# Performance work log

Hardware: AMD Instinct MI355X
Metric: run time of the kernel (lower is better)

Reference implementation:

```python
import jax, jax.numpy as jnp
import numpy as np


def setup_inputs() -> dict:
    key = jax.random.key(0)
    k1, k2 = jax.random.split(key)
    N, D, E = 16384, 4096, 64  # tokens, n_embd, n_exp
    x = jax.random.normal(k1, (N, D), dtype=jnp.float32)
    W = jax.random.normal(k2, (E, D), dtype=jnp.float32) * 0.02  # w_gate weight [n_exp, n_embd]
    return {"x": x, "W": W, "top_k": 4, "n_groups": 8, "n_limited_groups": 4}


def reference(x, W, top_k, n_groups, n_limited_groups):
    ROUTE_SCALE = 1.0
    N = x.shape[0]
    E = W.shape[0]
    exp_per_group = E // n_groups

    logits = x @ W.T                      # [N, E] gate linear (bias=False)
    scores = jax.nn.softmax(logits, -1)   # func == 'softmax'

    # group-limited routing: pick top n_limited_groups groups by max score (bias=False path)
    gs = scores.reshape(N, n_groups, exp_per_group)
    group_scores = gs.max(axis=-1)                             # [N, G]
    _, top_grp = jax.lax.top_k(group_scores, n_limited_groups)  # [N, L]
    selected = jnp.any(
        jnp.arange(n_groups)[None, None, :] == top_grp[:, :, None], axis=1
    )                                                           # [N, G] bool
    masked = jnp.where(selected[:, :, None], gs, -jnp.inf).reshape(N, E)

    # top-k experts over unmasked scores; weights are the gathered scores
    topk_vals, topk_idx = jax.lax.top_k(masked, top_k)          # [N, K]
    weights = (topk_vals * ROUTE_SCALE).astype(x.dtype)         # softmax -> no renorm

    # histc over expert ids
    counts = jnp.zeros((E,), jnp.int32).at[topk_idx.reshape(-1)].add(1)
    return weights, topk_idx, counts
```

## Files before the change

kernel.cpp:

```cpp
#include <hip/hip_runtime.h>
#include <math.h>

#define NTOK 16384
#define DDIM 4096
#define NEXP 64
#define KTOP 4

#define SPLITK 16
#define KPER (DDIM / SPLITK)
#define BK 32
#define NSTG (KPER / BK)
#define WROWS 16
#define NWAVE 4
#define TPB (WROWS * NWAVE)
#define NBLK ((NTOK / TPB) * SPLITK)

typedef __attribute__((ext_vector_type(8))) short short8;
typedef __attribute__((ext_vector_type(4))) float f32x4;


__device__ __forceinline__ unsigned short f2bf_rtn(float x) {
    unsigned int b = __float_as_uint(x);
    return (unsigned short)((b + 0x7FFFu + ((b >> 16) & 1u)) >> 16);
}
__device__ __forceinline__ float bf2f(unsigned short h) {
    return __uint_as_float(((unsigned int)h) << 16);
}
__device__ __forceinline__ short8 mk8(unsigned int a, unsigned int b,
                                      unsigned int c, unsigned int d) {
    union { unsigned int u[4]; short8 s; } p;
    p.u[0] = a; p.u[1] = b; p.u[2] = c; p.u[3] = d;
    return p.s;
}
__device__ __forceinline__ void gl2lds16(const void* g, void* l) {
    __builtin_amdgcn_global_load_lds(
        (const __attribute__((address_space(1))) unsigned int*)g,
        (__attribute__((address_space(3))) unsigned int*)l, 16, 0, 0);
}

__global__ __launch_bounds__(256) void prep_kernel(
    const float* __restrict__ W, unsigned short* __restrict__ Whi,
    unsigned short* __restrict__ Wlo, float* __restrict__ counts)
{
    int idx = blockIdx.x * 256 + threadIdx.x;
    float x = W[idx];
    unsigned short h = f2bf_rtn(x);
    float lo = x - bf2f(h);
    Whi[idx] = h;
    Wlo[idx] = f2bf_rtn(lo);
    if (blockIdx.x == 0 && threadIdx.x < NEXP) counts[threadIdx.x] = 0.0f;
}

__global__ __launch_bounds__(256, 2) void gemm_kernel(
    const float* __restrict__ X, const unsigned short* __restrict__ Whi,
    const unsigned short* __restrict__ Wlo, float* __restrict__ part)
{
    __shared__ unsigned short sH[NEXP * KPER];
    __shared__ unsigned short sL[NEXP * KPER];
    __shared__ float sXa[NWAVE][2][WROWS * BK];

    const int tid  = threadIdx.x;
    const int lane = tid & 63;
    const int w    = tid >> 6;
    const int tb   = blockIdx.x >> 4;
    const int s    = blockIdx.x & 15;
    const int kbase = s * KPER;
    const int wtok  = tb * TPB + w * WROWS;

    #pragma unroll
    for (int i = 0; i < 8; ++i) {
        const int g  = i * 256 + tid;
        const int e  = g >> 5;
        const int p  = g & 31;
        const int gb = (i * 256 + (tid >> 6) * 64) * 8;
        const size_t src = (size_t)e * DDIM + kbase + ((p ^ (e & 7)) << 3);
        gl2lds16(Whi + src, &sH[gb]);
        gl2lds16(Wlo + src, &sL[gb]);
    }

    const int xrow = (lane >> 3);
    const int xp   = lane & 7;
    const float* xsrc0 = X + (size_t)(wtok + xrow) * DDIM + kbase
                       + ((xp ^ (xrow & 7)) << 2);
    const float* xsrc1 = X + (size_t)(wtok + 8 + xrow) * DDIM + kbase
                       + ((xp ^ ((xrow + 8) & 7)) << 2);
    float* const xb0 = &sXa[w][0][0];
    float* const xb1 = &sXa[w][1][0];

#define ISSUE_X(buf, st)                                                    \
    {                                                                       \
        gl2lds16(xsrc0 + (st) * BK, (buf));                                 \
        gl2lds16(xsrc1 + (st) * BK, (buf) + 256);                           \
    }

    ISSUE_X(xb0, 0)
    ISSUE_X(xb1, 1)
    __syncthreads();

    const int fr = lane & 15;
    const int fg = lane >> 4;
    const int xkey = fr & 7;

    f32x4 acc[4];
    #pragma unroll
    for (int ng = 0; ng < 4; ++ng) acc[ng] = (f32x4){0.f, 0.f, 0.f, 0.f};

    #pragma unroll
    for (int st = 0; st < NSTG; ++st) {
        if (st < NSTG - 1) {
            asm volatile("s_waitcnt vmcnt(2)" ::: "memory");
        } else {
            asm volatile("s_waitcnt vmcnt(0)" ::: "memory");
        }
        __builtin_amdgcn_sched_barrier(0);

        const float* cx = (st & 1) ? xb1 : xb0;

        const float4 qa = *(const float4*)&cx[fr * BK + (((fg * 2    ) ^ xkey) << 2)];
        const float4 qb = *(const float4*)&cx[fr * BK + (((fg * 2 + 1) ^ xkey) << 2)];

        const unsigned int u0 = __float_as_uint(qa.x), u1 = __float_as_uint(qa.y);
        const unsigned int u2 = __float_as_uint(qa.z), u3 = __float_as_uint(qa.w);
        const unsigned int u4 = __float_as_uint(qb.x), u5 = __float_as_uint(qb.y);
        const unsigned int u6 = __float_as_uint(qb.z), u7 = __float_as_uint(qb.w);
        const short8 ahi = mk8((u0 >> 16) | (u1 & 0xFFFF0000u),
                               (u2 >> 16) | (u3 & 0xFFFF0000u),
                               (u4 >> 16) | (u5 & 0xFFFF0000u),
                               (u6 >> 16) | (u7 & 0xFFFF0000u));
        const float l0 = qa.x - __uint_as_float(u0 & 0xFFFF0000u);
        const float l1 = qa.y - __uint_as_float(u1 & 0xFFFF0000u);
        const float l2 = qa.z - __uint_as_float(u2 & 0xFFFF0000u);
        const float l3 = qa.w - __uint_as_float(u3 & 0xFFFF0000u);
        const float l4 = qb.x - __uint_as_float(u4 & 0xFFFF0000u);
        const float l5 = qb.y - __uint_as_float(u5 & 0xFFFF0000u);
        const float l6 = qb.z - __uint_as_float(u6 & 0xFFFF0000u);
        const float l7 = qb.w - __uint_as_float(u7 & 0xFFFF0000u);
        const short8 alo = mk8(
            (__float_as_uint(l0) >> 16) | (__float_as_uint(l1) & 0xFFFF0000u),
            (__float_as_uint(l2) >> 16) | (__float_as_uint(l3) & 0xFFFF0000u),
            (__float_as_uint(l4) >> 16) | (__float_as_uint(l5) & 0xFFFF0000u),
            (__float_as_uint(l6) >> 16) | (__float_as_uint(l7) & 0xFFFF0000u));

        #pragma unroll
        for (int ng = 0; ng < 4; ++ng) {
            const int e  = ng * 16 + fr;
            const int so = e * KPER + (((st * 4 + fg) ^ xkey) << 3);
            const short8 bh = *(const short8*)&sH[so];
            const short8 bl = *(const short8*)&sL[so];
            acc[ng] = __builtin_amdgcn_mfma_f32_16x16x32_bf16(ahi, bh, acc[ng], 0, 0, 0);
            acc[ng] = __builtin_amdgcn_mfma_f32_16x16x32_bf16(ahi, bl, acc[ng], 0, 0, 0);
            acc[ng] = __builtin_amdgcn_mfma_f32_16x16x32_bf16(alo, bh, acc[ng], 0, 0, 0);
        }

        if (st + 2 < NSTG) {
            asm volatile("s_waitcnt lgkmcnt(0)" ::: "memory");
            __builtin_amdgcn_sched_barrier(0);
            float* nb = (st & 1) ? xb1 : xb0;
            ISSUE_X(nb, st + 2)
        }
    }
#undef ISSUE_X

    #pragma unroll
    for (int r = 0; r < 4; ++r) {
        const int n = wtok + fg * 4 + r;
        float* __restrict__ pp = part + ((size_t)n * SPLITK + s) * NEXP;
        #pragma unroll
        for (int ng = 0; ng < 4; ++ng)
            pp[ng * 16 + fr] = acc[ng][r];
    }
}

__global__ __launch_bounds__(256) void route_kernel(
    const float* __restrict__ part, float* __restrict__ outW,
    float* __restrict__ outI, float* __restrict__ counts)
{
    __shared__ int hist[NEXP];
    const int tid = threadIdx.x;
    if (tid < NEXP) hist[tid] = 0;
    __syncthreads();

    const int lane = tid & 63;
    const int wv   = tid >> 6;
    const int tok_base = blockIdx.x * 32 + wv * 8;

    for (int t = 0; t < 8; ++t) {
        const int n = tok_base + t;
        float L = 0.0f;
        #pragma unroll
        for (int s = 0; s < SPLITK; ++s)
            L += part[((size_t)n * SPLITK + s) * NEXP + lane];

        float m = L;
        #pragma unroll
        for (int off = 32; off > 0; off >>= 1) m = fmaxf(m, __shfl_xor(m, off));
        float p = expf(L - m);
        float ssum = p;
        #pragma unroll
        for (int off = 32; off > 0; off >>= 1) ssum += __shfl_xor(ssum, off);
        const float score = p / ssum;

        float gm = score;
        gm = fmaxf(gm, __shfl_xor(gm, 1));
        gm = fmaxf(gm, __shfl_xor(gm, 2));
        gm = fmaxf(gm, __shfl_xor(gm, 4));

        float ga[8];
        #pragma unroll
        for (int g = 0; g < 8; ++g) ga[g] = __shfl(gm, g * 8);
        unsigned selmask = 0u;
        #pragma unroll
        for (int r = 0; r < 4; ++r) {
            float best = -INFINITY; int bg = 0;
            #pragma unroll
            for (int g = 0; g < 8; ++g) {
                bool taken  = (selmask >> g) & 1u;
                bool better = (!taken) && (ga[g] > best);
                bg   = better ? g : bg;
                best = better ? ga[g] : best;
            }
            selmask |= (1u << bg);
        }

        float ms = ((selmask >> (lane >> 3)) & 1u) ? score : -INFINITY;
        float wk[4]; int wi[4];
        #pragma unroll
        for (int r = 0; r < 4; ++r) {
            float v = ms; int ix = lane;
            #pragma unroll
            for (int off = 32; off > 0; off >>= 1) {
                float vo = __shfl_xor(v, off);
                int   io = __shfl_xor(ix, off);
                if (vo > v || (vo == v && io < ix)) { v = vo; ix = io; }
            }
            wk[r] = v; wi[r] = ix;
            if (lane == ix) ms = -INFINITY;
        }

        if (lane == 0) {
            *(float4*)&outW[(size_t)n * 4] = make_float4(wk[0], wk[1], wk[2], wk[3]);
            *(float4*)&outI[(size_t)n * 4] =
                make_float4((float)wi[0], (float)wi[1], (float)wi[2], (float)wi[3]);
            atomicAdd(&hist[wi[0]], 1);
            atomicAdd(&hist[wi[1]], 1);
            atomicAdd(&hist[wi[2]], 1);
            atomicAdd(&hist[wi[3]], 1);
        }
    }

    __syncthreads();
    if (tid < NEXP) atomicAdd(&counts[tid], (float)hist[tid]);
}

extern "C" void kernel_launch(void* const* d_in, const int* in_sizes, int n_in,
                              void* d_out, int out_size, void* d_ws, size_t ws_size,
                              hipStream_t stream) {
    const float* X = (const float*)d_in[0];
    const float* W = (const float*)d_in[1];

    float* outW   = (float*)d_out;
    float* outI   = outW + (size_t)NTOK * KTOP;
    float* counts = outW + (size_t)2 * NTOK * KTOP;

    float*          part = (float*)d_ws;
    unsigned short* Whi  = (unsigned short*)(part + (size_t)NTOK * SPLITK * NEXP);
    unsigned short* Wlo  = Whi + (size_t)NEXP * DDIM;

    prep_kernel<<<(NEXP * DDIM) / 256, 256, 0, stream>>>(W, Whi, Wlo, counts);
    gemm_kernel<<<NBLK, 256, 0, stream>>>(X, Whi, Wlo, part);
    route_kernel<<<NTOK / 32, 256, 0, stream>>>(part, outW, outI, counts);
}
```

Measured before the change: 115.1 us.

## Stream W slices per stage with triple-buffered block-shared LDS and fewer split-K partitions

Instead of preloading a whole 64x256 W slice (hi/lo bf16) into LDS per block, the GEMM now streams 32-wide W and X tiles per stage into a three-slot ring shared by all 8 waves, with a block barrier each stage. Split-K drops from 16 to 4, and blocks grow to 512 threads covering 128 tokens. This cuts LDS footprint and the prologue load, shrinks the partial-sum buffer and route-kernel reduction, and amortizes each W tile over more tokens. In exchange it adds a per-stage __syncthreads-style barrier and relies on hand-tuned vmcnt counts being correct.

New measurement: 108.2 us. -6.0%, faster.

```diff
diff --git a/kernel.cpp b/kernel.cpp
--- a/kernel.cpp
+++ b/kernel.cpp
@@ -6,13 +6,11 @@
 #define NEXP 64
 #define KTOP 4
 
-#define SPLITK 16
+#define SPLITK 4
 #define KPER (DDIM / SPLITK)
 #define BK 32
 #define NSTG (KPER / BK)
-#define WROWS 16
-#define NWAVE 4
-#define TPB (WROWS * NWAVE)
+#define TPB 128
 #define NBLK ((NTOK / TPB) * SPLITK)
 
 typedef __attribute__((ext_vector_type(8))) short short8;
@@ -51,55 +49,52 @@
     if (blockIdx.x == 0 && threadIdx.x < NEXP) counts[threadIdx.x] = 0.0f;
 }
 
-__global__ __launch_bounds__(256, 2) void gemm_kernel(
+__global__ __launch_bounds__(512, 4) void gemm_kernel(
     const float* __restrict__ X, const unsigned short* __restrict__ Whi,
     const unsigned short* __restrict__ Wlo, float* __restrict__ part)
 {
-    __shared__ unsigned short sH[NEXP * KPER];
-    __shared__ unsigned short sL[NEXP * KPER];
-    __shared__ float sXa[NWAVE][2][WROWS * BK];
+    __shared__ float          sX[3][TPB * BK];
+    __shared__ unsigned short sH[3][NEXP * BK];
+    __shared__ unsigned short sL[3][NEXP * BK];
 
     const int tid  = threadIdx.x;
     const int lane = tid & 63;
     const int w    = tid >> 6;
-    const int tb   = blockIdx.x >> 4;
-    const int s    = blockIdx.x & 15;
+    const int tb   = blockIdx.x >> 2;
+    const int s    = blockIdx.x & 3;
     const int kbase = s * KPER;
-    const int wtok  = tb * TPB + w * WROWS;
-
-    #pragma unroll
-    for (int i = 0; i < 8; ++i) {
-        const int g  = i * 256 + tid;
-        const int e  = g >> 5;
-        const int p  = g & 31;
-        const int gb = (i * 256 + (tid >> 6) * 64) * 8;
-        const size_t src = (size_t)e * DDIM + kbase + ((p ^ (e & 7)) << 3);
-        gl2lds16(Whi + src, &sH[gb]);
-        gl2lds16(Wlo + src, &sL[gb]);
-    }
-
-    const int xrow = (lane >> 3);
-    const int xp   = lane & 7;
-    const float* xsrc0 = X + (size_t)(wtok + xrow) * DDIM + kbase
-                       + ((xp ^ (xrow & 7)) << 2);
-    const float* xsrc1 = X + (size_t)(wtok + 8 + xrow) * DDIM + kbase
-                       + ((xp ^ ((xrow + 8) & 7)) << 2);
-    float* const xb0 = &sXa[w][0][0];
-    float* const xb1 = &sXa[w][1][0];
-
-#define ISSUE_X(buf, st)                                                    \
+    const int tok0 = tb * TPB;
+
+    const int r0 = (w * 2    ) * 8 + (lane >> 3);
+    const int r1 = (w * 2 + 1) * 8 + (lane >> 3);
+    const int xp = lane & 7;
+    const float* xsrc0 = X + (size_t)(tok0 + r0) * DDIM + kbase + ((xp ^ (r0 & 7)) << 2);
+    const float* xsrc1 = X + (size_t)(tok0 + r1) * DDIM + kbase + ((xp ^ (r1 & 7)) << 2);
+    const int xdst0 = (w * 2    ) * 256;
+    const int xdst1 = (w * 2 + 1) * 256;
+
+    const unsigned short* const wtab_src = (w < 4) ? Whi : Wlo;
+    const int eb = w & 3;
+    const int we = eb * 16 + (lane & 15);
+    const unsigned short* wsrc = wtab_src + (size_t)we * DDIM + kbase + (lane >> 4) * 8;
+    const int wdst = eb * 512 + lane * 8;
+    unsigned short (* const wtab_dst)[NEXP * BK] = (w < 4) ? sH : sL;
+
+#define ISSUE(st_, slot_)                                                   \
     {                                                                       \
-        gl2lds16(xsrc0 + (st) * BK, (buf));                                 \
-        gl2lds16(xsrc1 + (st) * BK, (buf) + 256);                           \
-    }
-
-    ISSUE_X(xb0, 0)
-    ISSUE_X(xb1, 1)
+        gl2lds16(xsrc0 + (st_) * BK, &sX[slot_][xdst0]);                    \
+        gl2lds16(xsrc1 + (st_) * BK, &sX[slot_][xdst1]);                    \
+        gl2lds16(wsrc  + (st_) * BK, &wtab_dst[slot_][wdst]);               \
+    }
+
+    ISSUE(0, 0)
+    ISSUE(1, 1)
     __syncthreads();
 
     const int fr = lane & 15;
     const int fg = lane >> 4;
-    const int xkey = fr & 7;
+    const int aoff = (w * 16 + fr) * BK;
+    const int akey = fr & 7;
 
     f32x4 acc[4];
     #pragma unroll
@@ -107,17 +102,12 @@
 
     #pragma unroll
     for (int st = 0; st < NSTG; ++st) {
-        if (st < NSTG - 1) {
-            asm volatile("s_waitcnt vmcnt(2)" ::: "memory");
-        } else {
-            asm volatile("s_waitcnt vmcnt(0)" ::: "memory");
-        }
-        __builtin_amdgcn_sched_barrier(0);
-
-        const float* cx = (st & 1) ? xb1 : xb0;
-
-        const float4 qa = *(const float4*)&cx[fr * BK + (((fg * 2    ) ^ xkey) << 2)];
-        const float4 qb = *(const float4*)&cx[fr * BK + (((fg * 2 + 1) ^ xkey) << 2)];
+        const int slot = st % 3;
+
+        if (st + 2 < NSTG) ISSUE(st + 2, (st + 2) % 3)
+
+        const float4 qa = *(const float4*)&sX[slot][aoff + (((fg * 2    ) ^ akey) << 2)];
+        const float4 qb = *(const float4*)&sX[slot][aoff + (((fg * 2 + 1) ^ akey) << 2)];
 
         const unsigned int u0 = __float_as_uint(qa.x), u1 = __float_as_uint(qa.y);
         const unsigned int u2 = __float_as_uint(qa.z), u3 = __float_as_uint(qa.w);
@@ -143,27 +133,29 @@
 
         #pragma unroll
         for (int ng = 0; ng < 4; ++ng) {
-            const int e  = ng * 16 + fr;
-            const int so = e * KPER + (((st * 4 + fg) ^ xkey) << 3);
-            const short8 bh = *(const short8*)&sH[so];
-            const short8 bl = *(const short8*)&sL[so];
+            const int bo = ng * 512 + fg * 128 + fr * 8;
+            const short8 bh = *(const short8*)&sH[slot][bo];
+            const short8 bl = *(const short8*)&sL[slot][bo];
             acc[ng] = __builtin_amdgcn_mfma_f32_16x16x32_bf16(ahi, bh, acc[ng], 0, 0, 0);
             acc[ng] = __builtin_amdgcn_mfma_f32_16x16x32_bf16(ahi, bl, acc[ng], 0, 0, 0);
             acc[ng] = __builtin_amdgcn_mfma_f32_16x16x32_bf16(alo, bh, acc[ng], 0, 0, 0);
         }
 
-        if (st + 2 < NSTG) {
-            asm volatile("s_waitcnt lgkmcnt(0)" ::: "memory");
+        if (st < NSTG - 1) {
+            if (st < NSTG - 2) {
+                asm volatile("s_waitcnt vmcnt(3)" ::: "memory");
+            } else {
+                asm volatile("s_waitcnt vmcnt(0)" ::: "memory");
+            }
             __builtin_amdgcn_sched_barrier(0);
-            float* nb = (st & 1) ? xb1 : xb0;
-            ISSUE_X(nb, st + 2)
-        }
-    }
-#undef ISSUE_X
+            __builtin_amdgcn_s_barrier();
+        }
+    }
+#undef ISSUE
 
     #pragma unroll
     for (int r = 0; r < 4; ++r) {
-        const int n = wtok + fg * 4 + r;
+        const int n = tok0 + w * 16 + fg * 4 + r;
         float* __restrict__ pp = part + ((size_t)n * SPLITK + s) * NEXP;
         #pragma unroll
         for (int ng = 0; ng < 4; ++ng)
@@ -267,6 +259,6 @@
     unsigned short* Wlo  = Whi + (size_t)NEXP * DDIM;
 
     prep_kernel<<<(NEXP * DDIM) / 256, 256, 0, stream>>>(W, Whi, Wlo, counts);
-    gemm_kernel<<<NBLK, 256, 0, stream>>>(X, Whi, Wlo, part);
+    gemm_kernel<<<NBLK, 512, 0, stream>>>(X, Whi, Wlo, part);
     route_kernel<<<NTOK / 32, 256, 0, stream>>>(part, outW, outI, counts);
 }
```
